# Optimization experiments

Measured on AMD Instinct MI355X. Metric: run time of the kernel, lower is better.

## Reference

```python
import jax, jax.numpy as jnp
import numpy as np

SOW_INIT = 1e-10  # sum_of_weights_initial_value
EPS = 1e-8       # torch.nn.CosineSimilarity default eps


def setup_inputs() -> dict:
    key = jax.random.key(0)
    k1, k2, k3 = jax.random.split(key, 3)
    input_image = jax.random.normal(k1, (1, 3, 224, 224), dtype=jnp.float32)
    masks = jax.random.uniform(k2, (1000, 224, 224), dtype=jnp.float32)
    # Linear encoder: flattened image [3*224*224] -> feature dim 128
    W = jax.random.normal(k3, (3, 224, 224, 128), dtype=jnp.float32) * 0.01
    return {"input_image": input_image, "masks": masks, "W": W}


def reference(input_image, masks, W):
    img = input_image[0]  # [3, H, W]
    # Encoder applied to (img * mask): rep_n = sum_chw (img*mask)[c,h,w] * W[c,h,w,f]
    # Precompute A[h,w,f] = sum_c img[c,h,w] * W[c,h,w,f] so masked reps never
    # materialize the [N,3,H,W] masked-image tensor.
    A = jnp.einsum('chw,chwf->hwf', img, W)          # [H, W, F]
    rep0 = jnp.sum(A, axis=(0, 1))                   # unmasked representation [F]
    reps = jnp.einsum('nhw,hwf->nf', masks, A)       # masked representations [N, F]

    # Cosine similarity (dim=1), clamped norms as in torch
    n0 = jnp.maximum(jnp.linalg.norm(rep0), EPS)
    nr = jnp.maximum(jnp.linalg.norm(reps, axis=1), EPS)
    sims = (reps @ rep0) / (nr * n0)                 # [N]

    H, Wd = masks.shape[1], masks.shape[2]
    imp0 = jnp.zeros((H, Wd), dtype=jnp.float32)
    unc0 = jnp.zeros((H, Wd), dtype=jnp.float32)
    sow0 = jnp.full((H, Wd), SOW_INIT, dtype=jnp.float32)

    def step(carry, inp):
        imp, unc, sow = carry
        m, s = inp  # mask [H,W], similarity scalar
        sow = sow + m
        prev = imp
        imp = imp + m * (s - imp) / sow
        unc = unc + (s - imp) * (s - prev) * m
        return (imp, unc, sow), None

    (imp, unc, sow), _ = jax.lax.scan(step, (imp0, unc0, sow0), (masks, sims))
    return jnp.stack([imp, unc, sow])  # [3, H, W]
```

## Files before the change

### kernel.cpp

```cpp
#include <hip/hip_runtime.h>
#include <hip/hip_bf16.h>
#include <stdint.h>

#define HWN 50176
#define NM  1000
#define FD  128
#define NSPLIT 49
#define KSTEPS 32
#define NSCAN 20
#define NPB 50

typedef __attribute__((ext_vector_type(8))) short short8;
typedef __attribute__((ext_vector_type(4))) float f32x4;

__device__ __forceinline__ unsigned short f2bf(float x) {
    union { float f; unsigned u; } v; v.f = x;
    unsigned r = v.u + 0x7FFFu + ((v.u >> 16) & 1u);
    return (unsigned short)(r >> 16);
}

#define AS1(p) ((const __attribute__((address_space(1))) unsigned int*)(p))
#define AS3(p) ((__attribute__((address_space(3))) unsigned int*)(p))

__global__ __launch_bounds__(256) void k_encode(const float* __restrict__ img,
                                                const float* __restrict__ Wt,
                                                unsigned short* __restrict__ Bpack,
                                                float* __restrict__ rep0part)
{
    const int t = threadIdx.x;
    const int f = t & 127;
    const int kt = blockIdx.x * 2 + (t >> 7);
    const int hw0 = kt * 32;
    float vals[32];
    float rsum = 0.f;
#pragma unroll
    for (int e = 0; e < 32; ++e) {
        const int hw = hw0 + e;
        float a = img[hw] * Wt[(size_t)hw * FD + f];
        a = fmaf(img[HWN + hw],     Wt[(size_t)(HWN + hw) * FD + f], a);
        a = fmaf(img[2 * HWN + hw], Wt[(size_t)(2 * HWN + hw) * FD + f], a);
        vals[e] = a;
        rsum += a;
    }
    char* tile = (char*)Bpack + (size_t)kt * 8192;
#pragma unroll
    for (int j = 0; j < 4; ++j) {
        short8 pk;
#pragma unroll
        for (int e = 0; e < 8; ++e) pk[e] = (short)f2bf(vals[j * 8 + e]);
        *reinterpret_cast<short8*>(tile + j * 2048 + (((f + j) & 127) << 4)) = pk;
    }
    __shared__ float red[256];
    red[t] = rsum;
    __syncthreads();
    if (t < 128) rep0part[(size_t)blockIdx.x * 128 + f] = red[t] + red[t + 128];
}

__global__ __launch_bounds__(256) void k_rep0red(const float* __restrict__ rep0part,
                                                 float* __restrict__ rep0)
{
    const int f = blockIdx.x;
    float s = 0.f;
    for (int b = threadIdx.x; b < 784; b += 256) s += rep0part[(size_t)b * 128 + f];
    __shared__ float red[256];
    red[threadIdx.x] = s;
    __syncthreads();
    for (int o = 128; o > 0; o >>= 1) {
        if (threadIdx.x < o) red[threadIdx.x] += red[threadIdx.x + o];
        __syncthreads();
    }
    if (threadIdx.x == 0) rep0[f] = red[0];
}

__global__ __launch_bounds__(256, 3) void k_gemm(const float* __restrict__ masks,
                                                 const unsigned short* __restrict__ Bpack,
                                                 float* __restrict__ partial)
{
    __shared__ __align__(16) char lds[3][16384];

    const int t = threadIdx.x;
    const int wv = t >> 6, lane = t & 63;
    const int lrow = lane & 15, kg = lane >> 4;
    const int mtile = blockIdx.x, split = blockIdx.y;
    const int n0 = mtile * 64;

    const int s1 = 256 + t;
    const int ar0 = t >> 3, ar1 = s1 >> 3;
    const int ac0 = (t & 7) ^ (ar0 & 7);
    const int ac1 = (t & 7) ^ (ar1 & 7);
    int arow0 = n0 + ar0; if (arow0 >= NM) arow0 = NM - 1;
    int arow1 = n0 + ar1; if (arow1 >= NM) arow1 = NM - 1;
    const float* aSrc0 = masks + (size_t)arow0 * HWN + split * 1024 + ac0 * 4;
    const float* aSrc1 = masks + (size_t)arow1 * HWN + split * 1024 + ac1 * 4;
    const char*  bSrc  = (const char*)Bpack + (size_t)split * KSTEPS * 8192 + t * 16;

    const int r = wv * 16 + lrow;
    const int ao0 = r * 128 + (((2 * kg)     ^ (r & 7)) << 4);
    const int ao1 = r * 128 + ((((2 * kg)+1) ^ (r & 7)) << 4);
    int bo[8];
#pragma unroll
    for (int ft = 0; ft < 8; ++ft)
        bo[ft] = 8192 + kg * 2048 + (((ft * 16 + lrow + kg) & 127) << 4);

    f32x4 acc[8];
#pragma unroll
    for (int i = 0; i < 8; ++i) acc[i] = f32x4{0.f, 0.f, 0.f, 0.f};

#define STAGE(KS, BUF) do {                                                             \
        char* base_ = &lds[BUF][0];                                                     \
        __builtin_amdgcn_global_load_lds(AS1(aSrc0 + (KS) * 32), AS3(base_ + t * 16), 16, 0, 0);          \
        __builtin_amdgcn_global_load_lds(AS1(aSrc1 + (KS) * 32), AS3(base_ + 4096 + t * 16), 16, 0, 0);   \
        __builtin_amdgcn_global_load_lds(AS1(bSrc + (size_t)(KS) * 8192),        AS3(base_ + 8192 + t * 16), 16, 0, 0);        \
        __builtin_amdgcn_global_load_lds(AS1(bSrc + (size_t)(KS) * 8192 + 4096), AS3(base_ + 12288 + t * 16), 16, 0, 0);       \
    } while (0)

    STAGE(0, 0);
    STAGE(1, 1);
    asm volatile("s_waitcnt vmcnt(4)" ::: "memory");
    __builtin_amdgcn_s_barrier();
    __builtin_amdgcn_sched_barrier(0);

    int cur = 0, stg = 2;
    for (int ks = 0; ks < KSTEPS; ++ks) {
        if (ks + 2 < KSTEPS) STAGE(ks + 2, stg);

        const char* A = &lds[cur][0];
        const f32x4 alo = *reinterpret_cast<const f32x4*>(A + ao0);
        const f32x4 ahi = *reinterpret_cast<const f32x4*>(A + ao1);
        union { short8 s; __hip_bfloat162 h[4]; } apk;
        apk.h[0] = __float22bfloat162_rn(float2{alo[0], alo[1]});
        apk.h[1] = __float22bfloat162_rn(float2{alo[2], alo[3]});
        apk.h[2] = __float22bfloat162_rn(float2{ahi[0], ahi[1]});
        apk.h[3] = __float22bfloat162_rn(float2{ahi[2], ahi[3]});
        short8 bfv[8];
#pragma unroll
        for (int ft = 0; ft < 8; ++ft)
            bfv[ft] = *reinterpret_cast<const short8*>(A + bo[ft]);

        asm volatile("s_waitcnt lgkmcnt(0)" ::: "memory");
        __builtin_amdgcn_sched_barrier(0);
        __builtin_amdgcn_s_setprio(1);
#pragma unroll
        for (int ft = 0; ft < 8; ++ft)
            acc[ft] = __builtin_amdgcn_mfma_f32_16x16x32_bf16(apk.s, bfv[ft], acc[ft], 0, 0, 0);
        __builtin_amdgcn_s_setprio(0);
        __builtin_amdgcn_sched_barrier(0);

        if (ks < KSTEPS - 2)       asm volatile("s_waitcnt vmcnt(4)" ::: "memory");
        else if (ks == KSTEPS - 2) asm volatile("s_waitcnt vmcnt(0)" ::: "memory");
        if (ks < KSTEPS - 1) {
            __builtin_amdgcn_s_barrier();
            __builtin_amdgcn_sched_barrier(0);
        }
        cur = (cur + 1 == 3) ? 0 : cur + 1;
        stg = (stg + 1 == 3) ? 0 : stg + 1;
    }
#undef STAGE

    const int crow = n0 + wv * 16 + (kg << 2);
    float* pb = partial + ((size_t)split * 1024 + crow) * FD + lrow;
#pragma unroll
    for (int ft = 0; ft < 8; ++ft)
#pragma unroll
        for (int rr = 0; rr < 4; ++rr)
            __builtin_nontemporal_store(acc[ft][rr], pb + (size_t)rr * FD + ft * 16);
}

__global__ __launch_bounds__(128) void k_sims(const float* __restrict__ partial,
                                              const float* __restrict__ rep0,
                                              float* __restrict__ sims)
{
    const int n = blockIdx.x;
    const int f = threadIdx.x;
    float rsum = 0.f;
    for (int s = 0; s < NSPLIT; ++s)
        rsum += __builtin_nontemporal_load(partial + ((size_t)s * 1024 + n) * FD + f);
    const float r0 = rep0[f];
    __shared__ float red0[128], red1[128], red2[128];
    red0[f] = rsum * r0;
    red1[f] = rsum * rsum;
    red2[f] = r0 * r0;
    __syncthreads();
    for (int o = 64; o > 0; o >>= 1) {
        if (f < o) {
            red0[f] += red0[f + o];
            red1[f] += red1[f + o];
            red2[f] += red2[f + o];
        }
        __syncthreads();
    }
    if (f == 0) {
        const float nr = fmaxf(sqrtf(red1[0]), 1e-8f);
        const float nz = fmaxf(sqrtf(red2[0]), 1e-8f);
        sims[n] = red0[0] / (nr * nz);
    }
}

__global__ __launch_bounds__(256) void k_colsums(const float* __restrict__ masks,
                                                 const float* __restrict__ sims,
                                                 float* __restrict__ Spart)
{
    __shared__ float s1v[NPB], s2v[NPB];
    const int t = threadIdx.x;
    const int split = blockIdx.y;
    if (t < NPB) {
        const float s = sims[split * NPB + t];
        s1v[t] = s;
        s2v[t] = s * s;
    }
    __syncthreads();
    const int pix = (blockIdx.x * 256 + t) * 4;
    const float* mp = masks + (size_t)split * NPB * HWN + pix;
    f32x4 s0 = {0.f,0.f,0.f,0.f}, s1 = s0, s2 = s0;
#pragma unroll 5
    for (int i = 0; i < NPB; ++i) {
        const f32x4 m = *reinterpret_cast<const f32x4*>(mp + (size_t)i * HWN);
        const float a = s1v[i], b = s2v[i];
        s0 += m;
#pragma unroll
        for (int e = 0; e < 4; ++e) {
            s1[e] = fmaf(m[e], a, s1[e]);
            s2[e] = fmaf(m[e], b, s2[e]);
        }
    }
    float* sp = Spart + (size_t)split * 3 * HWN + pix;
    __builtin_nontemporal_store(s0, reinterpret_cast<f32x4*>(sp));
    __builtin_nontemporal_store(s1, reinterpret_cast<f32x4*>(sp + HWN));
    __builtin_nontemporal_store(s2, reinterpret_cast<f32x4*>(sp + 2 * HWN));
}

__global__ __launch_bounds__(256) void k_final(const float* __restrict__ Spart,
                                               float* __restrict__ out)
{
    const int pix = (blockIdx.x * 256 + threadIdx.x) * 4;
    f32x4 s0 = {0.f,0.f,0.f,0.f}, s1 = s0, s2 = s0;
#pragma unroll 4
    for (int sp = 0; sp < NSCAN; ++sp) {
        const float* p = Spart + (size_t)sp * 3 * HWN + pix;
        s0 += __builtin_nontemporal_load(reinterpret_cast<const f32x4*>(p));
        s1 += __builtin_nontemporal_load(reinterpret_cast<const f32x4*>(p + HWN));
        s2 += __builtin_nontemporal_load(reinterpret_cast<const f32x4*>(p + 2 * HWN));
    }
    f32x4 imp, unc, sow;
#pragma unroll
    for (int e = 0; e < 4; ++e) {
        sow[e] = 1e-10f + s0[e];
        imp[e] = s1[e] / sow[e];
        unc[e] = fmaf(-imp[e], s1[e], s2[e]);
    }
    *reinterpret_cast<f32x4*>(out + pix) = imp;
    *reinterpret_cast<f32x4*>(out + HWN + pix) = unc;
    *reinterpret_cast<f32x4*>(out + 2 * HWN + pix) = sow;
}

extern "C" void kernel_launch(void* const* d_in, const int* in_sizes, int n_in,
                              void* d_out, int out_size, void* d_ws, size_t ws_size,
                              hipStream_t stream) {
    const float* img   = (const float*)d_in[0];
    const float* masks = (const float*)d_in[1];
    const float* Wt    = (const float*)d_in[2];
    float* out = (float*)d_out;

    char* ws = (char*)d_ws;
    unsigned short* Bpack = (unsigned short*)ws;
    float* partial  = (float*)(ws + 12845056);
    float* rep0part = partial;
    float* rep0     = (float*)(ws + 38535168);
    float* sims     = (float*)(ws + 38535680);
    float* Spart    = (float*)ws;

    hipLaunchKernelGGL(k_encode,  dim3(784), dim3(256), 0, stream, img, Wt, Bpack, rep0part);
    hipLaunchKernelGGL(k_rep0red, dim3(128), dim3(256), 0, stream, rep0part, rep0);
    hipLaunchKernelGGL(k_gemm,    dim3(16, NSPLIT), dim3(256), 0, stream, masks, Bpack, partial);
    hipLaunchKernelGGL(k_sims,    dim3(NM), dim3(128), 0, stream, partial, rep0, sims);
    hipLaunchKernelGGL(k_colsums, dim3(49, NSCAN), dim3(256), 0, stream, masks, sims, Spart);
    hipLaunchKernelGGL(k_final,   dim3(49), dim3(256), 0, stream, Spart, out);
}
```

Measured before the change: 131.1 us.

## Load mask A-tiles directly into registers and shrink LDS to B-only buffers

The GEMM kernel now loads the fp32 mask rows straight from global memory into registers, prefetched two steps ahead, rather than staging them through LDS. Only the bf16 B tiles use the LDS triple buffer, with a new XOR-swizzled packing layout matching the encode kernel's write pattern. The smaller LDS footprint lets the launch bound rise to four blocks per CU. The grid is flattened to 1D with a block-index swizzle that groups splits and mtiles for locality, and the W loads in encode become nontemporal. In exchange it needs more registers for the prefetched A values and relies on per-lane 16B global loads being well coalesced.

New measurement: 123.2 us, median of 2. -6.0%, faster.

```diff
diff --git a/kernel.cpp b/kernel.cpp
--- a/kernel.cpp
+++ b/kernel.cpp
@@ -36,9 +36,9 @@
 #pragma unroll
     for (int e = 0; e < 32; ++e) {
         const int hw = hw0 + e;
-        float a = img[hw] * Wt[(size_t)hw * FD + f];
-        a = fmaf(img[HWN + hw],     Wt[(size_t)(HWN + hw) * FD + f], a);
-        a = fmaf(img[2 * HWN + hw], Wt[(size_t)(2 * HWN + hw) * FD + f], a);
+        float a = img[hw] * __builtin_nontemporal_load(Wt + (size_t)hw * FD + f);
+        a = fmaf(img[HWN + hw],     __builtin_nontemporal_load(Wt + (size_t)(HWN + hw) * FD + f), a);
+        a = fmaf(img[2 * HWN + hw], __builtin_nontemporal_load(Wt + (size_t)(2 * HWN + hw) * FD + f), a);
         vals[e] = a;
         rsum += a;
     }
@@ -48,7 +48,8 @@
         short8 pk;
 #pragma unroll
         for (int e = 0; e < 8; ++e) pk[e] = (short)f2bf(vals[j * 8 + e]);
-        *reinterpret_cast<short8*>(tile + j * 2048 + (((f + j) & 127) << 4)) = pk;
+        const int slot = (f * 4 + j) ^ ((f >> 1) & 3);
+        *reinterpret_cast<short8*>(tile + (slot << 4)) = pk;
     }
     __shared__ float red[256];
     red[t] = rsum;
@@ -72,70 +73,83 @@
     if (threadIdx.x == 0) rep0[f] = red[0];
 }
 
-__global__ __launch_bounds__(256, 3) void k_gemm(const float* __restrict__ masks,
+__global__ __launch_bounds__(256, 4) void k_gemm(const float* __restrict__ masks,
                                                  const unsigned short* __restrict__ Bpack,
                                                  float* __restrict__ partial)
 {
-    __shared__ __align__(16) char lds[3][16384];
+    __shared__ __align__(16) char Bs[3][8192];
 
     const int t = threadIdx.x;
     const int wv = t >> 6, lane = t & 63;
     const int lrow = lane & 15, kg = lane >> 4;
-    const int mtile = blockIdx.x, split = blockIdx.y;
+
+    const int bid = blockIdx.x;
+    const int swz = (bid & 7) * 98 + (bid >> 3);
+    const int split = swz >> 4, mtile = swz & 15;
     const int n0 = mtile * 64;
 
-    const int s1 = 256 + t;
-    const int ar0 = t >> 3, ar1 = s1 >> 3;
-    const int ac0 = (t & 7) ^ (ar0 & 7);
-    const int ac1 = (t & 7) ^ (ar1 & 7);
-    int arow0 = n0 + ar0; if (arow0 >= NM) arow0 = NM - 1;
-    int arow1 = n0 + ar1; if (arow1 >= NM) arow1 = NM - 1;
-    const float* aSrc0 = masks + (size_t)arow0 * HWN + split * 1024 + ac0 * 4;
-    const float* aSrc1 = masks + (size_t)arow1 * HWN + split * 1024 + ac1 * 4;
-    const char*  bSrc  = (const char*)Bpack + (size_t)split * KSTEPS * 8192 + t * 16;
-
-    const int r = wv * 16 + lrow;
-    const int ao0 = r * 128 + (((2 * kg)     ^ (r & 7)) << 4);
-    const int ao1 = r * 128 + ((((2 * kg)+1) ^ (r & 7)) << 4);
+    int row = n0 + wv * 16 + lrow;
+    if (row >= NM) row = NM - 1;
+    const float* aSrc = masks + (size_t)row * HWN + split * 1024 + kg * 8;
+    const char*  bSrc = (const char*)Bpack + (size_t)split * (KSTEPS * 8192) + t * 16;
+
     int bo[8];
 #pragma unroll
-    for (int ft = 0; ft < 8; ++ft)
-        bo[ft] = 8192 + kg * 2048 + (((ft * 16 + lrow + kg) & 127) << 4);
+    for (int ft = 0; ft < 8; ++ft) {
+        const int f = ft * 16 + lrow;
+        bo[ft] = ((f * 4 + kg) ^ ((f >> 1) & 3)) << 4;
+    }
 
     f32x4 acc[8];
 #pragma unroll
     for (int i = 0; i < 8; ++i) acc[i] = f32x4{0.f, 0.f, 0.f, 0.f};
 
-#define STAGE(KS, BUF) do {                                                             \
-        char* base_ = &lds[BUF][0];                                                     \
-        __builtin_amdgcn_global_load_lds(AS1(aSrc0 + (KS) * 32), AS3(base_ + t * 16), 16, 0, 0);          \
-        __builtin_amdgcn_global_load_lds(AS1(aSrc1 + (KS) * 32), AS3(base_ + 4096 + t * 16), 16, 0, 0);   \
-        __builtin_amdgcn_global_load_lds(AS1(bSrc + (size_t)(KS) * 8192),        AS3(base_ + 8192 + t * 16), 16, 0, 0);        \
-        __builtin_amdgcn_global_load_lds(AS1(bSrc + (size_t)(KS) * 8192 + 4096), AS3(base_ + 12288 + t * 16), 16, 0, 0);       \
+    f32x4 aA0, aA1, aB0, aB1, aC0, aC1;
+
+#define STAGE(KS, BUFOFF) do {                                                                     \
+        __builtin_amdgcn_global_load_lds(AS1(bSrc + (size_t)(KS) * 8192),        AS3(&Bs[0][0] + (BUFOFF) + ((t & 255) * 16)), 16, 0, 0); \
+        __builtin_amdgcn_global_load_lds(AS1(bSrc + (size_t)(KS) * 8192 + 4096), AS3(&Bs[0][0] + (BUFOFF) + 4096 + ((t & 255) * 16)), 16, 0, 0); \
     } while (0)
 
+    __builtin_amdgcn_sched_barrier(0);
     STAGE(0, 0);
-    STAGE(1, 1);
-    asm volatile("s_waitcnt vmcnt(4)" ::: "memory");
-    __builtin_amdgcn_s_barrier();
+    aA0 = *reinterpret_cast<const f32x4*>(aSrc);
+    aA1 = *reinterpret_cast<const f32x4*>(aSrc + 4);
     __builtin_amdgcn_sched_barrier(0);
-
-    int cur = 0, stg = 2;
+    STAGE(1, 8192);
+    aB0 = *reinterpret_cast<const f32x4*>(aSrc + 32);
+    aB1 = *reinterpret_cast<const f32x4*>(aSrc + 36);
+    __builtin_amdgcn_sched_barrier(0);
+
+    int boff_c = 0;
     for (int ks = 0; ks < KSTEPS; ++ks) {
-        if (ks + 2 < KSTEPS) STAGE(ks + 2, stg);
-
-        const char* A = &lds[cur][0];
-        const f32x4 alo = *reinterpret_cast<const f32x4*>(A + ao0);
-        const f32x4 ahi = *reinterpret_cast<const f32x4*>(A + ao1);
+        const int boff_s = (boff_c + 16384 >= 24576) ? (boff_c + 16384 - 24576) : (boff_c + 16384);
+        if (ks + 2 < KSTEPS) {
+            __builtin_amdgcn_sched_barrier(0);
+            STAGE(ks + 2, boff_s);
+            aC0 = *reinterpret_cast<const f32x4*>(aSrc + (ks + 2) * 32);
+            aC1 = *reinterpret_cast<const f32x4*>(aSrc + (ks + 2) * 32 + 4);
+            __builtin_amdgcn_sched_barrier(0);
+            asm volatile("s_waitcnt vmcnt(8)" ::: "memory");
+        } else if (ks == KSTEPS - 2) {
+            asm volatile("s_waitcnt vmcnt(4)" ::: "memory");
+        } else {
+            asm volatile("s_waitcnt vmcnt(0)" ::: "memory");
+        }
+        __builtin_amdgcn_s_barrier();
+        __builtin_amdgcn_sched_barrier(0);
+
+        const char* B = &Bs[0][0] + boff_c;
+        short8 bfv[8];
+#pragma unroll
+        for (int ft = 0; ft < 8; ++ft)
+            bfv[ft] = *reinterpret_cast<const short8*>(B + bo[ft]);
+
         union { short8 s; __hip_bfloat162 h[4]; } apk;
-        apk.h[0] = __float22bfloat162_rn(float2{alo[0], alo[1]});
-        apk.h[1] = __float22bfloat162_rn(float2{alo[2], alo[3]});
-        apk.h[2] = __float22bfloat162_rn(float2{ahi[0], ahi[1]});
-        apk.h[3] = __float22bfloat162_rn(float2{ahi[2], ahi[3]});
-        short8 bfv[8];
-#pragma unroll
-        for (int ft = 0; ft < 8; ++ft)
-            bfv[ft] = *reinterpret_cast<const short8*>(A + bo[ft]);
+        apk.h[0] = __float22bfloat162_rn(float2{aA0[0], aA0[1]});
+        apk.h[1] = __float22bfloat162_rn(float2{aA0[2], aA0[3]});
+        apk.h[2] = __float22bfloat162_rn(float2{aA1[0], aA1[1]});
+        apk.h[3] = __float22bfloat162_rn(float2{aA1[2], aA1[3]});
 
         asm volatile("s_waitcnt lgkmcnt(0)" ::: "memory");
         __builtin_amdgcn_sched_barrier(0);
@@ -145,15 +159,12 @@
             acc[ft] = __builtin_amdgcn_mfma_f32_16x16x32_bf16(apk.s, bfv[ft], acc[ft], 0, 0, 0);
         __builtin_amdgcn_s_setprio(0);
         __builtin_amdgcn_sched_barrier(0);
-
-        if (ks < KSTEPS - 2)       asm volatile("s_waitcnt vmcnt(4)" ::: "memory");
-        else if (ks == KSTEPS - 2) asm volatile("s_waitcnt vmcnt(0)" ::: "memory");
-        if (ks < KSTEPS - 1) {
+        if (ks + 1 < KSTEPS) {
             __builtin_amdgcn_s_barrier();
             __builtin_amdgcn_sched_barrier(0);
         }
-        cur = (cur + 1 == 3) ? 0 : cur + 1;
-        stg = (stg + 1 == 3) ? 0 : stg + 1;
+        aA0 = aB0; aA1 = aB1; aB0 = aC0; aB1 = aC1;
+        boff_c = (boff_c + 8192 >= 24576) ? 0 : (boff_c + 8192);
     }
 #undef STAGE
 
@@ -271,7 +282,7 @@
 
     hipLaunchKernelGGL(k_encode,  dim3(784), dim3(256), 0, stream, img, Wt, Bpack, rep0part);
     hipLaunchKernelGGL(k_rep0red, dim3(128), dim3(256), 0, stream, rep0part, rep0);
-    hipLaunchKernelGGL(k_gemm,    dim3(16, NSPLIT), dim3(256), 0, stream, masks, Bpack, partial);
+    hipLaunchKernelGGL(k_gemm,    dim3(784), dim3(256), 0, stream, masks, Bpack, partial);
     hipLaunchKernelGGL(k_sims,    dim3(NM), dim3(128), 0, stream, partial, rep0, sims);
     hipLaunchKernelGGL(k_colsums, dim3(49, NSCAN), dim3(256), 0, stream, masks, sims, Spart);
     hipLaunchKernelGGL(k_final,   dim3(49), dim3(256), 0, stream, Spart, out);
```
